# Performance work log

Measured on AMD Instinct MI355X. Metric: run time of the kernel, lower is better.

## Reference

```python
import jax, jax.numpy as jnp
import numpy as np

E, CAP, D, H = 8, 2048, 1024, 4096  # experts, capacity, model_dim, hidden

def setup_inputs() -> dict:
    key = jax.random.key(0)
    k = jax.random.split(key, 5)
    s1 = 1.0 / np.sqrt(D)
    s2 = 1.0 / np.sqrt(H)
    return {
        "x": jax.random.normal(k[0], (E, CAP, D), dtype=jnp.float32),
        "fc1_w": jax.random.uniform(k[1], (E, H, D), jnp.float32, -s1, s1),
        "fc1_b": jax.random.uniform(k[2], (E, H), jnp.float32, -s1, s1),
        "fc2_w": jax.random.uniform(k[3], (E, H, D), jnp.float32, -s2, s2),
        "fc2_b": jax.random.uniform(k[4], (E, D), jnp.float32, -s2, s2),
    }

def reference(x, fc1_w, fc1_b, fc2_w, fc2_b):
    # y = relu(x @ fc1_w^T + b1) @ fc2_w + b2, batched over experts e
    y = jnp.einsum('ecd,ehd->ech', x, fc1_w) + fc1_b[:, None, :]   # [E, CAP, H]
    y = jax.nn.relu(y)
    y = jnp.einsum('ech,ehd->ecd', y, fc2_w) + fc2_b[:, None, :]   # [E, CAP, D]
    return y
```

## Files before the change

### kernel.cpp

```cpp
#include <hip/hip_runtime.h>
#include <hip/hip_bf16.h>
#include <stdint.h>

#define E_    8
#define CAP_  2048
#define D_    1024
#define H_    4096

typedef unsigned short u16;
typedef __attribute__((ext_vector_type(8))) short bf16x8;
typedef __attribute__((ext_vector_type(4))) float f32x4;

__device__ __forceinline__ u16 f2bf(float f) {
    union { float f; unsigned int u; } v; v.f = f;
    unsigned int u = v.u;
    unsigned int r = (u + 0x7fffu + ((u >> 16) & 1u)) >> 16;
    return (u16)r;
}

__device__ __forceinline__ void gload_lds16(const void* g, void* l) {
    __builtin_amdgcn_global_load_lds(
        (const __attribute__((address_space(1))) unsigned int*)g,
        (__attribute__((address_space(3))) unsigned int*)l,
        16, 0, 0);
}

__global__ void cvt_f32_bf16(const float* __restrict__ in, u16* __restrict__ out, int n4) {
    int i = blockIdx.x * blockDim.x + threadIdx.x;
    if (i >= n4) return;
    const float4 v = ((const float4*)in)[i];
    ushort4 o;
    o.x = f2bf(v.x); o.y = f2bf(v.y); o.z = f2bf(v.z); o.w = f2bf(v.w);
    ((ushort4*)out)[i] = o;
}

__global__ void transpose_cvt(const float* __restrict__ in, u16* __restrict__ out) {
    __shared__ float t[32][33];
    const int e  = blockIdx.z;
    const int h0 = blockIdx.y * 32;
    const int d0 = blockIdx.x * 32;
    const float* I = in + (size_t)e * H_ * D_;
    u16* O = out + (size_t)e * D_ * H_;
    const int tx = threadIdx.x, ty = threadIdx.y;
    t[ty][tx] = I[(size_t)(h0 + ty) * D_ + d0 + tx];
    __syncthreads();
    O[(size_t)(d0 + ty) * H_ + h0 + tx] = f2bf(t[tx][ty]);
}

template<int EPI>
__global__ __launch_bounds__(512, 2) void gemm256(
    const u16* __restrict__ A, const u16* __restrict__ B,
    const float* __restrict__ bias, void* __restrict__ Cv,
    int M, int N, int K, int TM, int TN,
    size_t sA, size_t sB, size_t sBias, size_t sC)
{
    __shared__ __align__(16) u16 lds[2][2][2][128 * 64];

    const int nwg = gridDim.x;
    const int cpx = nwg >> 3;
    const int bid = blockIdx.x;
    const int wg  = (bid & 7) * cpx + (bid >> 3);
    const int tpe = TM * TN;
    const int e   = wg / tpe;
    const int rem = wg - e * tpe;
    const int tn  = rem / TM;
    const int tm  = rem - tn * TM;
    const int row0 = tm << 8;
    const int col0 = tn << 8;

    const u16* Ae = A + (size_t)e * sA;
    const u16* Be = B + (size_t)e * sB;

    const int tid  = threadIdx.x;
    const int lane = tid & 63;
    const int w    = tid >> 6;
    const int wr   = w >> 2;
    const int wc   = w & 3;
    const int wcH  = wc >> 1;
    const int wcL  = wc & 1;
    const int fr   = lane & 15;
    const int fq   = lane >> 4;
    const int cx   = (fq ^ (fr & 7)) << 4;
    const int lo0  = fr * 128 + cx;
    const int lo1  = fr * 128 + (cx ^ 64);
    const int sl   = lane ^ ((lane >> 3) & 7);
    const int NT   = K >> 6;

    f32x4 acc[8][4] = {};

    auto stageA = [&](int u, int hf) {
        if (u >= NT) return;
        u16* dst = &lds[u & 1][0][hf][0];
        const int k0 = u << 6;
        #pragma unroll
        for (int l = 0; l < 2; ++l) {
            const int bc = (w * 2 + l) << 6;
            const int a  = bc + sl;
            gload_lds16(Ae + (size_t)(row0 + (hf << 7) + (a >> 3)) * K + (k0 + ((a & 7) << 3)),
                        dst + bc * 8);
        }
    };
    auto stageB = [&](int u, int hf) {
        if (u >= NT) return;
        u16* dst = &lds[u & 1][1][hf][0];
        const int k0 = u << 6;
        #pragma unroll
        for (int l = 0; l < 2; ++l) {
            const int bc = (w * 2 + l) << 6;
            const int a  = bc + sl;
            gload_lds16(Be + (size_t)(col0 + (hf << 7) + (a >> 3)) * K + (k0 + ((a & 7) << 3)),
                        dst + bc * 8);
        }
    };

    stageB(0, 0); stageB(0, 1); stageA(0, 0); stageA(0, 1);
    stageB(1, 0); stageB(1, 1);
    asm volatile("s_waitcnt vmcnt(4)");
    __builtin_amdgcn_s_barrier();

    for (int t = 0; t < NT; ++t) {
        const int db = t & 1;
        const char* Ah = (const char*)&lds[db][0][wr][0];
        const char* Bh = (const char*)&lds[db][1][wcH][0];
        bf16x8 b[4][2];
        #pragma unroll
        for (int p = 0; p < 4; ++p) {
            if (p == 0) {
                #pragma unroll
                for (int n = 0; n < 4; ++n) {
                    b[n][0] = *(const bf16x8*)(Bh + wcL * 8192 + n * 2048 + lo0);
                    b[n][1] = *(const bf16x8*)(Bh + wcL * 8192 + n * 2048 + lo1);
                }
            }
            bf16x8 a[2][2];
            #pragma unroll
            for (int mm = 0; mm < 2; ++mm) {
                a[mm][0] = *(const bf16x8*)(Ah + (2 * p + mm) * 2048 + lo0);
                a[mm][1] = *(const bf16x8*)(Ah + (2 * p + mm) * 2048 + lo1);
            }
            if (p == 0)      stageA(t + 1, 0);
            else if (p == 1) stageA(t + 1, 1);
            else if (p == 2) stageB(t + 2, 0);
            else             stageB(t + 2, 1);

            __builtin_amdgcn_s_barrier();
            __builtin_amdgcn_s_setprio(1);
            #pragma unroll
            for (int kk = 0; kk < 2; ++kk)
                #pragma unroll
                for (int mm = 0; mm < 2; ++mm)
                    #pragma unroll
                    for (int n = 0; n < 4; ++n)
                        acc[2 * p + mm][n] = __builtin_amdgcn_mfma_f32_16x16x32_bf16(
                            a[mm][kk], b[n][kk], acc[2 * p + mm][n], 0, 0, 0);
            __builtin_amdgcn_s_setprio(0);
            if (p == 3) {
                if (t < NT - 2)       asm volatile("s_waitcnt vmcnt(4)");
                else if (t == NT - 2) asm volatile("s_waitcnt vmcnt(0)");
            }
            __builtin_amdgcn_s_barrier();
        }
    }

    const float* be = bias + (size_t)e * sBias;
    if (EPI == 0) {
        u16* cl = (u16*)&lds[0][0][0][0];
        __builtin_amdgcn_s_barrier();
        #pragma unroll
        for (int n = 0; n < 4; ++n) {
            const int ccol = wc * 64 + n * 16 + fr;
            const float bv = be[col0 + ccol];
            #pragma unroll
            for (int m = 0; m < 8; ++m) {
                const int crow = wr * 128 + m * 16 + fq * 4;
                #pragma unroll
                for (int i = 0; i < 4; ++i) {
                    float v = acc[m][n][i] + bv;
                    v = v > 0.f ? v : 0.f;
                    cl[(crow + i) * 256 + ccol] = f2bf(v);
                }
            }
        }
        __builtin_amdgcn_s_barrier();
        u16* Ce = (u16*)Cv + (size_t)e * sC;
        const int rr = tid >> 5;
        const int cc = (tid & 31) * 8;
        #pragma unroll
        for (int s = 0; s < 16; ++s) {
            const int row = s * 16 + rr;
            const float4 v = *(const float4*)&cl[row * 256 + cc];
            *(float4*)&Ce[(size_t)(row0 + row) * N + col0 + cc] = v;
        }
    } else {
        float* cf = (float*)&lds[0][0][0][0];
        float* Ce = (float*)Cv + (size_t)e * sC;
        #pragma unroll
        for (int p = 0; p < 2; ++p) {
            __builtin_amdgcn_s_barrier();
            #pragma unroll
            for (int n = 0; n < 4; ++n) {
                const int ccol = wc * 64 + n * 16 + fr;
                const float bv = be[col0 + ccol];
                #pragma unroll
                for (int mm = 0; mm < 4; ++mm) {
                    const int lrow = wr * 64 + mm * 16 + fq * 4;
                    #pragma unroll
                    for (int i = 0; i < 4; ++i)
                        cf[(lrow + i) * 256 + ccol] = acc[p * 4 + mm][n][i] + bv;
                }
            }
            __builtin_amdgcn_s_barrier();
            const int lr = tid >> 6;
            const int cc = (tid & 63) * 4;
            #pragma unroll
            for (int s = 0; s < 16; ++s) {
                const int lrow = s * 8 + lr;
                const int wrr  = lrow >> 6;
                const int rem2 = lrow & 63;
                const int grow = row0 + wrr * 128 + p * 64 + rem2;
                const float4 v = *(const float4*)&cf[lrow * 256 + cc];
                *(float4*)&Ce[(size_t)grow * N + col0 + cc] = v;
            }
        }
    }
}

extern "C" void kernel_launch(void* const* d_in, const int* in_sizes, int n_in,
                              void* d_out, int out_size, void* d_ws, size_t ws_size,
                              hipStream_t stream) {
    (void)in_sizes; (void)n_in; (void)out_size; (void)ws_size;
    const float* x     = (const float*)d_in[0];
    const float* fc1_w = (const float*)d_in[1];
    const float* fc1_b = (const float*)d_in[2];
    const float* fc2_w = (const float*)d_in[3];
    const float* fc2_b = (const float*)d_in[4];
    float* out = (float*)d_out;

    u16* xbf  = (u16*)d_ws;
    u16* w1bf = xbf  + (size_t)E_ * CAP_ * D_;
    u16* w2t  = w1bf + (size_t)E_ * H_ * D_;
    u16* y1   = w2t  + (size_t)E_ * D_ * H_;

    {
        int n4 = E_ * CAP_ * D_ / 4;
        cvt_f32_bf16<<<n4 / 256, 256, 0, stream>>>(x, xbf, n4);
    }
    {
        int n4 = E_ * H_ * D_ / 4;
        cvt_f32_bf16<<<n4 / 256, 256, 0, stream>>>(fc1_w, w1bf, n4);
    }
    transpose_cvt<<<dim3(D_ / 32, H_ / 32, E_), dim3(32, 32), 0, stream>>>(fc2_w, w2t);

    gemm256<0><<<dim3(E_ * (CAP_ / 256) * (H_ / 256)), 512, 0, stream>>>(
        xbf, w1bf, fc1_b, y1, CAP_, H_, D_, CAP_ / 256, H_ / 256,
        (size_t)CAP_ * D_, (size_t)H_ * D_, (size_t)H_, (size_t)CAP_ * H_);

    gemm256<1><<<dim3(E_ * (CAP_ / 256) * (D_ / 256)), 512, 0, stream>>>(
        y1, w2t, fc2_b, out, CAP_, D_, H_, CAP_ / 256, D_ / 256,
        (size_t)CAP_ * H_, (size_t)D_ * H_, (size_t)D_, (size_t)CAP_ * D_);
}
```

Measured before the change: 384.9 us.

## Drop a per-phase barrier in GEMM, precompute staging pointers, vectorize transpose

The GEMM main loop now issues one workgroup barrier per sub-phase instead of two. The B fragment reads are hoisted out of the phase loop, and global-to-LDS staging uses precomputed, incrementing pointers with a predicate in place of per-call address math and early returns. The redundant barrier before the epilogue is also removed. Separately, the fc2 transpose-convert kernel moves to 64x64 tiles with float4 loads and ushort4 stores to cut per-element memory transactions. The change leans on the remaining barriers to order LDS reuse, which risks races if the buffer reuse schedule has been misjudged.

```diff
diff --git a/kernel.cpp b/kernel.cpp
--- a/kernel.cpp
+++ b/kernel.cpp
@@ -35,16 +35,30 @@
 }
 
 __global__ void transpose_cvt(const float* __restrict__ in, u16* __restrict__ out) {
-    __shared__ float t[32][33];
+    __shared__ float t[64][69];
     const int e  = blockIdx.z;
-    const int h0 = blockIdx.y * 32;
-    const int d0 = blockIdx.x * 32;
+    const int h0 = blockIdx.y * 64;
+    const int d0 = blockIdx.x * 64;
     const float* I = in + (size_t)e * H_ * D_;
     u16* O = out + (size_t)e * D_ * H_;
-    const int tx = threadIdx.x, ty = threadIdx.y;
-    t[ty][tx] = I[(size_t)(h0 + ty) * D_ + d0 + tx];
+    const int tid = threadIdx.x;
+    const int r  = tid >> 4;
+    const int c  = (tid & 15) * 4;
+    #pragma unroll
+    for (int s = 0; s < 4; ++s) {
+        const int h = r + s * 16;
+        const float4 v = *(const float4*)&I[(size_t)(h0 + h) * D_ + d0 + c];
+        t[h][c] = v.x; t[h][c + 1] = v.y; t[h][c + 2] = v.z; t[h][c + 3] = v.w;
+    }
     __syncthreads();
-    O[(size_t)(d0 + ty) * H_ + h0 + tx] = f2bf(t[tx][ty]);
+    #pragma unroll
+    for (int s = 0; s < 4; ++s) {
+        const int d = r + s * 16;
+        ushort4 o;
+        o.x = f2bf(t[c + 0][d]); o.y = f2bf(t[c + 1][d]);
+        o.z = f2bf(t[c + 2][d]); o.w = f2bf(t[c + 3][d]);
+        *(ushort4*)&O[(size_t)(d0 + d) * H_ + h0 + c] = o;
+    }
 }
 
 template<int EPI>
@@ -86,35 +100,38 @@
     const int sl   = lane ^ ((lane >> 3) & 7);
     const int NT   = K >> 6;
 
+    const int srow = (w << 4) + (sl >> 3);
+    const int scol = (sl & 7) << 3;
+    const u16* pA[2][2];
+    const u16* pB[2][2];
+    #pragma unroll
+    for (int l = 0; l < 2; ++l)
+        #pragma unroll
+        for (int hf = 0; hf < 2; ++hf) {
+            pA[l][hf] = Ae + (size_t)(row0 + hf * 128 + srow + l * 8) * K + scol;
+            pB[l][hf] = Be + (size_t)(col0 + hf * 128 + srow + l * 8) * K + scol;
+        }
+
+    auto stageA = [&](int buf, int hf, bool pred) {
+        #pragma unroll
+        for (int l = 0; l < 2; ++l) {
+            if (pred) gload_lds16(pA[l][hf], &lds[buf][0][hf][(w * 2 + l) * 512]);
+            pA[l][hf] += 64;
+        }
+    };
+    auto stageB = [&](int buf, int hf, bool pred) {
+        #pragma unroll
+        for (int l = 0; l < 2; ++l) {
+            if (pred) gload_lds16(pB[l][hf], &lds[buf][1][hf][(w * 2 + l) * 512]);
+            pB[l][hf] += 64;
+        }
+    };
+
     f32x4 acc[8][4] = {};
 
-    auto stageA = [&](int u, int hf) {
-        if (u >= NT) return;
-        u16* dst = &lds[u & 1][0][hf][0];
-        const int k0 = u << 6;
-        #pragma unroll
-        for (int l = 0; l < 2; ++l) {
-            const int bc = (w * 2 + l) << 6;
-            const int a  = bc + sl;
-            gload_lds16(Ae + (size_t)(row0 + (hf << 7) + (a >> 3)) * K + (k0 + ((a & 7) << 3)),
-                        dst + bc * 8);
-        }
-    };
-    auto stageB = [&](int u, int hf) {
-        if (u >= NT) return;
-        u16* dst = &lds[u & 1][1][hf][0];
-        const int k0 = u << 6;
-        #pragma unroll
-        for (int l = 0; l < 2; ++l) {
-            const int bc = (w * 2 + l) << 6;
-            const int a  = bc + sl;
-            gload_lds16(Be + (size_t)(col0 + (hf << 7) + (a >> 3)) * K + (k0 + ((a & 7) << 3)),
-                        dst + bc * 8);
-        }
-    };
-
-    stageB(0, 0); stageB(0, 1); stageA(0, 0); stageA(0, 1);
-    stageB(1, 0); stageB(1, 1);
+    stageB(0, 0, true); stageB(0, 1, true);
+    stageA(0, 0, true); stageA(0, 1, true);
+    stageB(1, 0, true); stageB(1, 1, true);
     asm volatile("s_waitcnt vmcnt(4)");
     __builtin_amdgcn_s_barrier();
 
@@ -124,26 +141,23 @@
         const char* Bh = (const char*)&lds[db][1][wcH][0];
         bf16x8 b[4][2];
         #pragma unroll
+        for (int n = 0; n < 4; ++n) {
+            b[n][0] = *(const bf16x8*)(Bh + wcL * 8192 + n * 2048 + lo0);
+            b[n][1] = *(const bf16x8*)(Bh + wcL * 8192 + n * 2048 + lo1);
+        }
+        #pragma unroll
         for (int p = 0; p < 4; ++p) {
-            if (p == 0) {
-                #pragma unroll
-                for (int n = 0; n < 4; ++n) {
-                    b[n][0] = *(const bf16x8*)(Bh + wcL * 8192 + n * 2048 + lo0);
-                    b[n][1] = *(const bf16x8*)(Bh + wcL * 8192 + n * 2048 + lo1);
-                }
-            }
             bf16x8 a[2][2];
             #pragma unroll
             for (int mm = 0; mm < 2; ++mm) {
                 a[mm][0] = *(const bf16x8*)(Ah + (2 * p + mm) * 2048 + lo0);
                 a[mm][1] = *(const bf16x8*)(Ah + (2 * p + mm) * 2048 + lo1);
             }
-            if (p == 0)      stageA(t + 1, 0);
-            else if (p == 1) stageA(t + 1, 1);
-            else if (p == 2) stageB(t + 2, 0);
-            else             stageB(t + 2, 1);
-
-            __builtin_amdgcn_s_barrier();
+            if (p == 0)      stageA(db ^ 1, 0, t + 1 < NT);
+            else if (p == 1) stageA(db ^ 1, 1, t + 1 < NT);
+            else if (p == 2) stageB(db,     0, t + 2 < NT);
+            else             stageB(db,     1, t + 2 < NT);
+
             __builtin_amdgcn_s_setprio(1);
             #pragma unroll
             for (int kk = 0; kk < 2; ++kk)
@@ -165,7 +179,6 @@
     const float* be = bias + (size_t)e * sBias;
     if (EPI == 0) {
         u16* cl = (u16*)&lds[0][0][0][0];
-        __builtin_amdgcn_s_barrier();
         #pragma unroll
         for (int n = 0; n < 4; ++n) {
             const int ccol = wc * 64 + n * 16 + fr;
@@ -249,7 +262,7 @@
         int n4 = E_ * H_ * D_ / 4;
         cvt_f32_bf16<<<n4 / 256, 256, 0, stream>>>(fc1_w, w1bf, n4);
     }
-    transpose_cvt<<<dim3(D_ / 32, H_ / 32, E_), dim3(32, 32), 0, stream>>>(fc2_w, w2t);
+    transpose_cvt<<<dim3(D_ / 64, H_ / 64, E_), 256, 0, stream>>>(fc2_w, w2t);
 
     gemm256<0><<<dim3(E_ * (CAP_ / 256) * (H_ / 256)), 512, 0, stream>>>(
         xbf, w1bf, fc1_b, y1, CAP_, H_, D_, CAP_ / 256, H_ / 256,
```

Result: faster. 343.0 us (-10.9%).
